# Optimization experiments

Hardware: AMD Instinct MI355X
Metric: run time of the kernel (lower is better)

Reference implementation:

```python
import jax, jax.numpy as jnp
import numpy as np

N_NODES = 100_000
N_EDGES = 1_600_000
F_IN = 64
HID = 128
HEAD_H = 256
OUT = 32
N_GRAPHS = 512
NEG_SLOPE = 0.01  # torch.nn.LeakyReLU default


def _leaky(v):
    return jnp.where(v >= 0, v, NEG_SLOPE * v)


def _gine_layer(x, src, dst, edge_attr, We, be, Wn, bn, n_nodes):
    # GINEConv (eps=0): nn( x_i + sum_j relu(x_j + lin(edge_attr_ji)) )
    msg = jax.nn.relu(x[src] + edge_attr @ We + be)          # [E, in]
    agg = jax.ops.segment_sum(msg, dst, num_segments=n_nodes)  # [N, in]
    return (agg + x) @ Wn + bn                                # [N, hid]


def setup_inputs() -> dict:
    key = jax.random.key(0)
    ks = jax.random.split(key, 24)
    inp = {}
    inp["x"] = jax.random.normal(ks[0], (N_NODES, F_IN), dtype=jnp.float32)
    inp["edge_index"] = jax.random.randint(ks[1], (2, N_EDGES), 0, N_NODES, dtype=jnp.int32)
    inp["edge_attr"] = jax.random.normal(ks[2], (N_EDGES, 2), dtype=jnp.float32)
    inp["batch"] = jnp.sort(jax.random.randint(ks[3], (N_NODES,), 0, N_GRAPHS, dtype=jnp.int32))
    # GINE layers: edge lin (2 -> in) and nn Linear (in -> hid)
    dims = [F_IN, HID, HID]
    ki = 4
    for l, d_in in enumerate(dims):
        inp[f"We{l}"] = jax.random.normal(ks[ki], (2, d_in), dtype=jnp.float32) / np.sqrt(2.0); ki += 1
        inp[f"be{l}"] = jnp.zeros((d_in,), dtype=jnp.float32)
        inp[f"Wn{l}"] = jax.random.normal(ks[ki], (d_in, HID), dtype=jnp.float32) / np.sqrt(d_in); ki += 1
        inp[f"bn{l}"] = jnp.zeros((HID,), dtype=jnp.float32)
    # head MLP
    inp["Wh0"] = jax.random.normal(ks[ki], (HID, HEAD_H), dtype=jnp.float32) / np.sqrt(HID); ki += 1
    inp["bh0"] = jnp.zeros((HEAD_H,), dtype=jnp.float32)
    inp["Wh1"] = jax.random.normal(ks[ki], (HEAD_H, OUT), dtype=jnp.float32) / np.sqrt(HEAD_H); ki += 1
    inp["bh1"] = jnp.zeros((OUT,), dtype=jnp.float32)
    return inp


def reference(x, edge_index, edge_attr, batch,
              We0, be0, Wn0, bn0,
              We1, be1, Wn1, bn1,
              We2, be2, Wn2, bn2,
              Wh0, bh0, Wh1, bh1):
    src, dst = edge_index[0], edge_index[1]
    h = _leaky(_gine_layer(x, src, dst, edge_attr, We0, be0, Wn0, bn0, N_NODES))
    h = _leaky(_gine_layer(h, src, dst, edge_attr, We1, be1, Wn1, bn1, N_NODES))
    h = _leaky(_gine_layer(h, src, dst, edge_attr, We2, be2, Wn2, bn2, N_NODES))
    pooled = jax.ops.segment_sum(h, batch, num_segments=N_GRAPHS)  # [G, HID]
    h = _leaky(pooled @ Wh0 + bh0)
    return h @ Wh1 + bh1  # [G, OUT]
```

## Files before the change

kernel.cpp:

```cpp
#include <hip/hip_runtime.h>
#include <hip/hip_bf16.h>

#define N_NODES 100000
#define N_EDGES 1600000
#define F_IN 64
#define HID 128
#define HEAD_H 256
#define OUT_F 32
#define N_GRAPHS 512
#define NBK 98
#define SLOT 20480
#define BCHUNK 2048
#define NCHUNKS ((N_EDGES + BCHUNK - 1) / BCHUNK)

typedef float f2v __attribute__((ext_vector_type(2)));
typedef short bf16x8 __attribute__((ext_vector_type(8)));
typedef float f32x4 __attribute__((ext_vector_type(4)));

__device__ __forceinline__ float leaky(float v) {
    return v >= 0.f ? v : 0.01f * v;
}

__device__ __forceinline__ float bf2f(ushort u) {
    union { uint i; float f; } c; c.i = ((uint)u) << 16; return c.f;
}

__device__ __forceinline__ ushort f2bf(float f) {
    union { float f; uint i; } c; c.f = f;
    uint r = c.i + 0x7FFF + ((c.i >> 16) & 1);
    return (ushort)(r >> 16);
}

__global__ __launch_bounds__(256) void cast_kernel(const float* __restrict__ x,
                                                   ushort* __restrict__ xb, int n2) {
    int i = blockIdx.x * 256 + threadIdx.x;
    if (i < n2) {
        float2 v = ((const float2*)x)[i];
        uint u = (uint)f2bf(v.x) | ((uint)f2bf(v.y) << 16);
        ((uint*)xb)[i] = u;
    }
}

__global__ __launch_bounds__(256) void prep_wnT(const float* __restrict__ Wn0,
                                                const float* __restrict__ Wn1,
                                                const float* __restrict__ Wn2,
                                                ushort* __restrict__ w0T,
                                                ushort* __restrict__ w1T,
                                                ushort* __restrict__ w2T) {
    int id = blockIdx.x * 256 + threadIdx.x;
    if (id < 128 * 64) {
        int j = id / 64, k = id % 64;
        w0T[id] = f2bf(Wn0[k * 128 + j]);
    } else if (id < 128 * 64 + 128 * 128) {
        int t = id - 128 * 64; int j = t / 128, k = t % 128;
        w1T[t] = f2bf(Wn1[k * 128 + j]);
    } else if (id < 128 * 64 + 2 * 128 * 128) {
        int t = id - 128 * 64 - 128 * 128; int j = t / 128, k = t % 128;
        w2T[t] = f2bf(Wn2[k * 128 + j]);
    }
}


__global__ __launch_bounds__(128) void init_bcur(int* __restrict__ bcur) {
    int t = threadIdx.x;
    if (t < NBK) bcur[t] = t * SLOT;
}

__global__ __launch_bounds__(256) void bin_kernel(const int* __restrict__ src,
                                                  const int* __restrict__ dst,
                                                  const float2* __restrict__ ea,
                                                  int* __restrict__ bcur,
                                                  uint2* __restrict__ recs1) {
    __shared__ int hist[NBK], tmp[NBK], offs[NBK], cur[NBK], gbase[NBK];
    __shared__ uint2 stage[BCHUNK];
    __shared__ unsigned char sbid[BCHUNK];

    int tid = threadIdx.x;
    int e0 = blockIdx.x * BCHUNK;
    int nn = N_EDGES - e0; if (nn > BCHUNK) nn = BCHUNK;

    if (tid < NBK) hist[tid] = 0;
    __syncthreads();

    for (int i = tid; i < nn; i += 256) {
        atomicAdd(&hist[dst[e0 + i] >> 10], 1);
    }
    __syncthreads();

    if (tid < NBK) tmp[tid] = hist[tid];
    __syncthreads();
    for (int off = 1; off < NBK; off <<= 1) {
        int u = (tid < NBK && tid >= off) ? tmp[tid - off] : 0;
        __syncthreads();
        if (tid < NBK) tmp[tid] += u;
        __syncthreads();
    }
    if (tid < NBK) {
        int ex = tmp[tid] - hist[tid];
        offs[tid] = ex;
        cur[tid] = ex;
        gbase[tid] = (hist[tid] > 0) ? atomicAdd(&bcur[tid], hist[tid]) : 0;
    }
    __syncthreads();

    for (int i = tid; i < nn; i += 256) {
        int e = e0 + i;
        int d = dst[e];
        int b = d >> 10;
        int dloc = d & 1023;
        float2 a = ea[e];
        uint2 r;
        r.x = (uint)src[e] | ((uint)dloc << 22);
        r.y = (uint)f2bf(a.x) | ((uint)f2bf(a.y) << 16);
        int pos = atomicAdd(&cur[b], 1);
        stage[pos] = r;
        sbid[pos] = (unsigned char)b;
    }
    __syncthreads();

    for (int i = tid; i < nn; i += 256) {
        int b = sbid[i];
        recs1[gbase[b] + (i - offs[b])] = stage[i];
    }
}

__global__ __launch_bounds__(256) void order_kernel(const uint2* __restrict__ recs1,
                                                    const int* __restrict__ bcur,
                                                    int* __restrict__ rbeg,
                                                    int* __restrict__ rend,
                                                    uint2* __restrict__ recs2) {
    __shared__ int h[1024];
    __shared__ int ssum[256];
    int b = blockIdx.x;
    int tid = threadIdx.x;
    int base = b * SLOT;
    int end = bcur[b];

    for (int i = tid; i < 1024; i += 256) h[i] = 0;
    __syncthreads();

    for (int t = base + tid; t < end; t += 256) {
        atomicAdd(&h[recs1[t].x >> 22], 1);
    }
    __syncthreads();

    int i4 = tid * 4;
    int a0 = h[i4], a1 = h[i4 + 1], a2 = h[i4 + 2], a3 = h[i4 + 3];
    int s = a0 + a1 + a2 + a3;
    ssum[tid] = s;
    __syncthreads();
    for (int off = 1; off < 256; off <<= 1) {
        int u = (tid >= off) ? ssum[tid - off] : 0;
        __syncthreads();
        ssum[tid] += u;
        __syncthreads();
    }
    int pre = base + ssum[tid] - s;
    int c0 = pre, c1 = pre + a0, c2 = c1 + a1, c3 = c2 + a2;
    h[i4] = c0; h[i4 + 1] = c1; h[i4 + 2] = c2; h[i4 + 3] = c3;

    int n = (b << 10) + i4;
    if (n + 4 <= N_NODES) {
        *(int4*)(rbeg + n) = make_int4(c0, c1, c2, c3);
        *(int4*)(rend + n) = make_int4(c0 + a0, c1 + a1, c2 + a2, c3 + a3);
    } else {
        if (n + 0 < N_NODES) { rbeg[n + 0] = c0; rend[n + 0] = c0 + a0; }
        if (n + 1 < N_NODES) { rbeg[n + 1] = c1; rend[n + 1] = c1 + a1; }
        if (n + 2 < N_NODES) { rbeg[n + 2] = c2; rend[n + 2] = c2 + a2; }
        if (n + 3 < N_NODES) { rbeg[n + 3] = c3; rend[n + 3] = c3 + a3; }
    }
    __syncthreads();

    for (int t = base + tid; t < end; t += 256) {
        uint2 r = recs1[t];
        int pos = atomicAdd(&h[r.x >> 22], 1);
        recs2[pos] = make_uint2(r.x & 0x3FFFFFu, r.y);
    }
}


template <int K>
__global__ __launch_bounds__(256) void gine_fused(const ushort* __restrict__ xb,
                                                  const uint2* __restrict__ recs,
                                                  const int* __restrict__ rbeg,
                                                  const int* __restrict__ rend,
                                                  const float* __restrict__ We,
                                                  const float* __restrict__ be,
                                                  const ushort* __restrict__ wnT,
                                                  const float* __restrict__ bn,
                                                  ushort* __restrict__ hb) {
    __shared__ float tile[16 * K];
    __shared__ int node_ctr;
    int tid = threadIdx.x;
    int wave = tid >> 6;
    int lane = tid & 63;
    int n0 = blockIdx.x * 16;

    if (tid == 0) node_ctr = 0;
    __syncthreads();

    if constexpr (K == 128) {
        int j = lane * 2;
        f2v w0v = {We[j], We[j + 1]};
        f2v w1v = {We[128 + j], We[128 + j + 1]};
        f2v bbv = {be[j], be[j + 1]};
        const f2v zero = {0.f, 0.f};

        for (;;) {
            int q = 0;
            if (lane == 0) q = atomicAdd(&node_ctr, 1);
            q = __builtin_amdgcn_readfirstlane(q);
            if (q >= 16) break;
            int node = n0 + q;
            int rs = __builtin_amdgcn_readfirstlane(rbeg[node]);
            int re = __builtin_amdgcn_readfirstlane(rend[node]);
            f2v accv = {0.f, 0.f};

            auto proc = [&](uint2 r, uint u) {
                float ax = bf2f((ushort)(r.y & 0xFFFF));
                float ay = bf2f((ushort)(r.y >> 16));
                union { uint i; float f; } lo, hi;
                lo.i = u << 16;
                hi.i = u & 0xFFFF0000u;
                f2v xv = {lo.f, hi.f};
                f2v m = xv + bbv;
                m = ay * w1v + m;
                m = ax * w0v + m;
                m = __builtin_elementwise_max(m, zero);
                accv += m;
            };

            int t = rs;
            for (; t + 7 < re; t += 8) {
                uint2 r0 = recs[t];
                uint2 r1 = recs[t + 1];
                uint2 r2 = recs[t + 2];
                uint2 r3 = recs[t + 3];
                uint2 r4 = recs[t + 4];
                uint2 r5 = recs[t + 5];
                uint2 r6 = recs[t + 6];
                uint2 r7 = recs[t + 7];
                uint u0 = *(const uint*)(xb + (size_t)r0.x * 128 + j);
                uint u1 = *(const uint*)(xb + (size_t)r1.x * 128 + j);
                uint u2 = *(const uint*)(xb + (size_t)r2.x * 128 + j);
                uint u3 = *(const uint*)(xb + (size_t)r3.x * 128 + j);
                uint u4 = *(const uint*)(xb + (size_t)r4.x * 128 + j);
                uint u5 = *(const uint*)(xb + (size_t)r5.x * 128 + j);
                uint u6 = *(const uint*)(xb + (size_t)r6.x * 128 + j);
                uint u7 = *(const uint*)(xb + (size_t)r7.x * 128 + j);
                proc(r0, u0); proc(r1, u1); proc(r2, u2); proc(r3, u3);
                proc(r4, u4); proc(r5, u5); proc(r6, u6); proc(r7, u7);
            }
            for (; t + 3 < re; t += 4) {
                uint2 r0 = recs[t];
                uint2 r1 = recs[t + 1];
                uint2 r2 = recs[t + 2];
                uint2 r3 = recs[t + 3];
                uint u0 = *(const uint*)(xb + (size_t)r0.x * 128 + j);
                uint u1 = *(const uint*)(xb + (size_t)r1.x * 128 + j);
                uint u2 = *(const uint*)(xb + (size_t)r2.x * 128 + j);
                uint u3 = *(const uint*)(xb + (size_t)r3.x * 128 + j);
                proc(r0, u0); proc(r1, u1); proc(r2, u2); proc(r3, u3);
            }
            for (; t < re; t++) {
                uint2 r0 = recs[t];
                uint u0 = *(const uint*)(xb + (size_t)r0.x * 128 + j);
                proc(r0, u0);
            }

            int idx = (q * 128 + j) ^ ((q & 7) << 2);
            *(f2v*)&tile[idx] = accv;
        }
    } else {
        float w0 = We[lane], w1 = We[64 + lane], bb = be[lane];

        for (;;) {
            int q = 0;
            if (lane == 0) q = atomicAdd(&node_ctr, 1);
            q = __builtin_amdgcn_readfirstlane(q);
            if (q >= 16) break;
            int node = n0 + q;
            int rs = __builtin_amdgcn_readfirstlane(rbeg[node]);
            int re = __builtin_amdgcn_readfirstlane(rend[node]);
            float acc = 0.f;

            auto proc = [&](uint2 r, ushort u) {
                float ax = bf2f((ushort)(r.y & 0xFFFF));
                float ay = bf2f((ushort)(r.y >> 16));
                float m = bf2f(u) + bb;
                m = ay * w1 + m;
                m = ax * w0 + m;
                acc += fmaxf(m, 0.f);
            };

            int t = rs;
            for (; t + 7 < re; t += 8) {
                uint2 r0 = recs[t];
                uint2 r1 = recs[t + 1];
                uint2 r2 = recs[t + 2];
                uint2 r3 = recs[t + 3];
                uint2 r4 = recs[t + 4];
                uint2 r5 = recs[t + 5];
                uint2 r6 = recs[t + 6];
                uint2 r7 = recs[t + 7];
                ushort u0 = xb[(size_t)r0.x * 64 + lane];
                ushort u1 = xb[(size_t)r1.x * 64 + lane];
                ushort u2 = xb[(size_t)r2.x * 64 + lane];
                ushort u3 = xb[(size_t)r3.x * 64 + lane];
                ushort u4 = xb[(size_t)r4.x * 64 + lane];
                ushort u5 = xb[(size_t)r5.x * 64 + lane];
                ushort u6 = xb[(size_t)r6.x * 64 + lane];
                ushort u7 = xb[(size_t)r7.x * 64 + lane];
                proc(r0, u0); proc(r1, u1); proc(r2, u2); proc(r3, u3);
                proc(r4, u4); proc(r5, u5); proc(r6, u6); proc(r7, u7);
            }
            for (; t + 3 < re; t += 4) {
                uint2 r0 = recs[t];
                uint2 r1 = recs[t + 1];
                uint2 r2 = recs[t + 2];
                uint2 r3 = recs[t + 3];
                ushort u0 = xb[(size_t)r0.x * 64 + lane];
                ushort u1 = xb[(size_t)r1.x * 64 + lane];
                ushort u2 = xb[(size_t)r2.x * 64 + lane];
                ushort u3 = xb[(size_t)r3.x * 64 + lane];
                proc(r0, u0); proc(r1, u1); proc(r2, u2); proc(r3, u3);
            }
            for (; t < re; t++) {
                uint2 r0 = recs[t];
                ushort u0 = xb[(size_t)r0.x * 64 + lane];
                proc(r0, u0);
            }

            int idx = (q * 64 + lane) ^ ((q & 7) << 2);
            tile[idx] = acc;
        }
    }
    __syncthreads();

    {
        int l15 = lane & 15;
        int kgrp = (lane >> 4) * 8;
        int row = l15;
        int sw = (row & 7) << 2;
        int nt0 = wave * 2;
        int nt1 = nt0 + 1;
        float b0 = bn[nt0 * 16 + l15];
        float b1 = bn[nt1 * 16 + l15];
        f32x4 acc0 = {b0, b0, b0, b0};
        f32x4 acc1 = {b1, b1, b1, b1};

#pragma unroll
        for (int kk = 0; kk < K / 32; kk++) {
            int k0 = kk * 32 + kgrp;
            f32x4 p0 = *(const f32x4*)&tile[(row * K + k0) ^ sw];
            f32x4 p1 = *(const f32x4*)&tile[(row * K + k0 + 4) ^ sw];
            bf16x8 xr = *(const bf16x8*)(xb + (size_t)(n0 + row) * K + k0);
            bf16x8 a;
#pragma unroll
            for (int e = 0; e < 4; e++) {
                a[e]     = (short)f2bf(p0[e] + bf2f((ushort)xr[e]));
                a[e + 4] = (short)f2bf(p1[e] + bf2f((ushort)xr[e + 4]));
            }
            bf16x8 bf0 = *(const bf16x8*)(wnT + (size_t)(nt0 * 16 + l15) * K + k0);
            bf16x8 bf1 = *(const bf16x8*)(wnT + (size_t)(nt1 * 16 + l15) * K + k0);
            acc0 = __builtin_amdgcn_mfma_f32_16x16x32_bf16(a, bf0, acc0, 0, 0, 0);
            acc1 = __builtin_amdgcn_mfma_f32_16x16x32_bf16(a, bf1, acc1, 0, 0, 0);
        }

        int rbase = n0 + (lane >> 4) * 4;
#pragma unroll
        for (int r = 0; r < 4; r++) {
            hb[(size_t)(rbase + r) * HID + nt0 * 16 + l15] = f2bf(leaky(acc0[r]));
            hb[(size_t)(rbase + r) * HID + nt1 * 16 + l15] = f2bf(leaky(acc1[r]));
        }
    }
}

#define POOL_NPW 64
__global__ __launch_bounds__(256) void pool_kernel(const ushort* __restrict__ h,
                                                   const int* __restrict__ batch,
                                                   float* __restrict__ pooled) {
    int wid = (blockIdx.x * 256 + (int)threadIdx.x) >> 6;
    int lane = threadIdx.x & 63;
    int n0 = wid * POOL_NPW;
    if (n0 >= N_NODES) return;
    int n1 = n0 + POOL_NPW; if (n1 > N_NODES) n1 = N_NODES;

    int j = lane * 2;
    f2v acc = {0.f, 0.f};
    int g = __builtin_amdgcn_readfirstlane(batch[n0]);
    for (int i = n0; i < n1; i++) {
        int bg = __builtin_amdgcn_readfirstlane(batch[i]);
        if (bg != g) {
            atomicAdd(&pooled[g * HID + j], acc.x);
            atomicAdd(&pooled[g * HID + j + 1], acc.y);
            acc.x = 0.f; acc.y = 0.f;
            g = bg;
        }
        uint u = *(const uint*)(h + (size_t)i * HID + j);
        union { uint i; float f; } lo, hi;
        lo.i = u << 16;
        hi.i = u & 0xFFFF0000u;
        acc.x += lo.f;
        acc.y += hi.f;
    }
    atomicAdd(&pooled[g * HID + j], acc.x);
    atomicAdd(&pooled[g * HID + j + 1], acc.y);
}


__global__ __launch_bounds__(256) void head_kernel(const float* __restrict__ pooled,
                                                   const float* __restrict__ Wh0,
                                                   const float* __restrict__ bh0,
                                                   const float* __restrict__ Wh1,
                                                   const float* __restrict__ bh1,
                                                   float* __restrict__ out) {
    __shared__ float p[HID];
    __shared__ float hid[HEAD_H];
    int g = blockIdx.x;
    int t = threadIdx.x;
    if (t < HID) p[t] = pooled[g * HID + t];
    __syncthreads();
    float acc = bh0[t];
    for (int k = 0; k < HID; k++) acc += p[k] * Wh0[k * HEAD_H + t];
    hid[t] = leaky(acc);
    __syncthreads();
    if (t < OUT_F) {
        float o = bh1[t];
        for (int k = 0; k < HEAD_H; k++) o += hid[k] * Wh1[k * OUT_F + t];
        out[g * OUT_F + t] = o;
    }
}

extern "C" void kernel_launch(void* const* d_in, const int* in_sizes, int n_in,
                              void* d_out, int out_size, void* d_ws, size_t ws_size,
                              hipStream_t stream) {
    const float* x     = (const float*)d_in[0];
    const int*   ei    = (const int*)d_in[1];
    const float* ea    = (const float*)d_in[2];
    const int*   batch = (const int*)d_in[3];
    const float* We0 = (const float*)d_in[4];
    const float* be0 = (const float*)d_in[5];
    const float* Wn0 = (const float*)d_in[6];
    const float* bn0 = (const float*)d_in[7];
    const float* We1 = (const float*)d_in[8];
    const float* be1 = (const float*)d_in[9];
    const float* Wn1 = (const float*)d_in[10];
    const float* bn1 = (const float*)d_in[11];
    const float* We2 = (const float*)d_in[12];
    const float* be2 = (const float*)d_in[13];
    const float* Wn2 = (const float*)d_in[14];
    const float* bn2 = (const float*)d_in[15];
    const float* Wh0 = (const float*)d_in[16];
    const float* bh0 = (const float*)d_in[17];
    const float* Wh1 = (const float*)d_in[18];
    const float* bh1 = (const float*)d_in[19];

    const int* src = ei;
    const int* dst = ei + N_EDGES;

    char* ws = (char*)d_ws;
    size_t o = 0;
    uint2*  recs1 = (uint2*)(ws + o); o += (size_t)NBK * SLOT * 8;
    uint2*  recs2 = (uint2*)(ws + o); o += (size_t)NBK * SLOT * 8;
    ushort* xb0  = (ushort*)(ws + o); o += (size_t)N_NODES * 64 * 2;
    ushort* hbufA = (ushort*)(ws + o); o += (size_t)N_NODES * 128 * 2;
    ushort* hbufB = (ushort*)(ws + o); o += (size_t)N_NODES * 128 * 2;
    int*    rbeg = (int*)(ws + o);    o += 400384;
    int*    rend = (int*)(ws + o);    o += 400384;
    int*    bcur = (int*)(ws + o);    o += 4096;
    ushort* wnT0 = (ushort*)(ws + o); o += 128 * 64 * 2;
    ushort* wnT1 = (ushort*)(ws + o); o += 128 * 128 * 2;
    ushort* wnT2 = (ushort*)(ws + o); o += 128 * 128 * 2;
    float*  pooled = (float*)(ws + o); o += (size_t)N_GRAPHS * HID * 4;

    cast_kernel<<<(N_NODES * F_IN / 2 + 255) / 256, 256, 0, stream>>>(x, xb0, N_NODES * F_IN / 2);
    prep_wnT<<<160, 256, 0, stream>>>(Wn0, Wn1, Wn2, wnT0, wnT1, wnT2);

    init_bcur<<<1, 128, 0, stream>>>(bcur);
    bin_kernel<<<NCHUNKS, 256, 0, stream>>>(src, dst, (const float2*)ea, bcur, recs1);
    order_kernel<<<NBK, 256, 0, stream>>>(recs1, bcur, rbeg, rend, recs2);

    const int FUSED_BLOCKS = N_NODES / 16;

    gine_fused<64><<<FUSED_BLOCKS, 256, 0, stream>>>(xb0, recs2, rbeg, rend, We0, be0, wnT0, bn0, hbufA);
    gine_fused<128><<<FUSED_BLOCKS, 256, 0, stream>>>(hbufA, recs2, rbeg, rend, We1, be1, wnT1, bn1, hbufB);
    gine_fused<128><<<FUSED_BLOCKS, 256, 0, stream>>>(hbufB, recs2, rbeg, rend, We2, be2, wnT2, bn2, hbufA);

    hipMemsetAsync(pooled, 0, (size_t)N_GRAPHS * HID * sizeof(float), stream);
    pool_kernel<<<(N_NODES / POOL_NPW + 3) / 4, 256, 0, stream>>>(hbufA, batch, pooled);
    head_kernel<<<N_GRAPHS, 256, 0, stream>>>(pooled, Wh0, bh0, Wh1, bh1, (float*)d_out);
}
```

Baseline: 340.0 us.

## Merge setup kernels, vectorize binning loads, interleave row ranges, prefetch next node

Merges the cast and weight-transpose kernels into one launch and replaces the init_bcur kernel with a memset, storing bucket cursors as relative offsets. The binning kernel now loads dst, src and edge_attr as 4-wide vectors. Row begin and end are interleaved into one array, and the fused GINE kernels fetch the next work-stolen node's range before processing the current one. The aim is fewer launches and less memory latency, at the cost of more complex indexing and alignment assumptions on vector loads.

```diff
diff --git a/kernel.cpp b/kernel.cpp
--- a/kernel.cpp
+++ b/kernel.cpp
@@ -12,6 +12,7 @@
 #define SLOT 20480
 #define BCHUNK 2048
 #define NCHUNKS ((N_EDGES + BCHUNK - 1) / BCHUNK)
+#define CAST_BLOCKS (N_NODES * F_IN / 2 / 256)
 
 typedef float f2v __attribute__((ext_vector_type(2)));
 typedef short bf16x8 __attribute__((ext_vector_type(8)));
@@ -31,40 +32,35 @@
     return (ushort)(r >> 16);
 }
 
-__global__ __launch_bounds__(256) void cast_kernel(const float* __restrict__ x,
-                                                   ushort* __restrict__ xb, int n2) {
-    int i = blockIdx.x * 256 + threadIdx.x;
-    if (i < n2) {
+__global__ __launch_bounds__(256) void setup_kernel(const float* __restrict__ x,
+                                                    ushort* __restrict__ xb,
+                                                    const float* __restrict__ Wn0,
+                                                    const float* __restrict__ Wn1,
+                                                    const float* __restrict__ Wn2,
+                                                    ushort* __restrict__ w0T,
+                                                    ushort* __restrict__ w1T,
+                                                    ushort* __restrict__ w2T) {
+    int b = blockIdx.x;
+    if (b < CAST_BLOCKS) {
+        int i = b * 256 + threadIdx.x;
         float2 v = ((const float2*)x)[i];
         uint u = (uint)f2bf(v.x) | ((uint)f2bf(v.y) << 16);
         ((uint*)xb)[i] = u;
-    }
-}
-
-__global__ __launch_bounds__(256) void prep_wnT(const float* __restrict__ Wn0,
-                                                const float* __restrict__ Wn1,
-                                                const float* __restrict__ Wn2,
-                                                ushort* __restrict__ w0T,
-                                                ushort* __restrict__ w1T,
-                                                ushort* __restrict__ w2T) {
-    int id = blockIdx.x * 256 + threadIdx.x;
-    if (id < 128 * 64) {
-        int j = id / 64, k = id % 64;
-        w0T[id] = f2bf(Wn0[k * 128 + j]);
-    } else if (id < 128 * 64 + 128 * 128) {
-        int t = id - 128 * 64; int j = t / 128, k = t % 128;
-        w1T[t] = f2bf(Wn1[k * 128 + j]);
-    } else if (id < 128 * 64 + 2 * 128 * 128) {
-        int t = id - 128 * 64 - 128 * 128; int j = t / 128, k = t % 128;
-        w2T[t] = f2bf(Wn2[k * 128 + j]);
-    }
-}
-
-
-__global__ __launch_bounds__(128) void init_bcur(int* __restrict__ bcur) {
-    int t = threadIdx.x;
-    if (t < NBK) bcur[t] = t * SLOT;
-}
+    } else {
+        int id = (b - CAST_BLOCKS) * 256 + threadIdx.x;
+        if (id < 128 * 64) {
+            int j = id / 64, k = id % 64;
+            w0T[id] = f2bf(Wn0[k * 128 + j]);
+        } else if (id < 128 * 64 + 128 * 128) {
+            int t = id - 128 * 64; int j = t / 128, k = t % 128;
+            w1T[t] = f2bf(Wn1[k * 128 + j]);
+        } else if (id < 128 * 64 + 2 * 128 * 128) {
+            int t = id - 128 * 64 - 128 * 128; int j = t / 128, k = t % 128;
+            w2T[t] = f2bf(Wn2[k * 128 + j]);
+        }
+    }
+}
+
 
 __global__ __launch_bounds__(256) void bin_kernel(const int* __restrict__ src,
                                                   const int* __restrict__ dst,
@@ -82,8 +78,12 @@
     if (tid < NBK) hist[tid] = 0;
     __syncthreads();
 
-    for (int i = tid; i < nn; i += 256) {
-        atomicAdd(&hist[dst[e0 + i] >> 10], 1);
+    for (int i0 = tid * 4; i0 < nn; i0 += 1024) {
+        int4 d4 = *(const int4*)(dst + e0 + i0);
+        atomicAdd(&hist[d4.x >> 10], 1);
+        atomicAdd(&hist[d4.y >> 10], 1);
+        atomicAdd(&hist[d4.z >> 10], 1);
+        atomicAdd(&hist[d4.w >> 10], 1);
     }
     __syncthreads();
 
@@ -99,22 +99,30 @@
         int ex = tmp[tid] - hist[tid];
         offs[tid] = ex;
         cur[tid] = ex;
-        gbase[tid] = (hist[tid] > 0) ? atomicAdd(&bcur[tid], hist[tid]) : 0;
-    }
-    __syncthreads();
-
-    for (int i = tid; i < nn; i += 256) {
-        int e = e0 + i;
-        int d = dst[e];
-        int b = d >> 10;
-        int dloc = d & 1023;
-        float2 a = ea[e];
-        uint2 r;
-        r.x = (uint)src[e] | ((uint)dloc << 22);
-        r.y = (uint)f2bf(a.x) | ((uint)f2bf(a.y) << 16);
-        int pos = atomicAdd(&cur[b], 1);
-        stage[pos] = r;
-        sbid[pos] = (unsigned char)b;
+        gbase[tid] = (hist[tid] > 0) ? (tid * SLOT + atomicAdd(&bcur[tid], hist[tid])) : 0;
+    }
+    __syncthreads();
+
+    for (int i0 = tid * 4; i0 < nn; i0 += 1024) {
+        int e = e0 + i0;
+        int4 d4 = *(const int4*)(dst + e);
+        int4 s4 = *(const int4*)(src + e);
+        float4 ea01 = *(const float4*)(ea + e);
+        float4 ea23 = *(const float4*)(ea + e + 2);
+#pragma unroll
+        for (int k = 0; k < 4; k++) {
+            int d = (k == 0) ? d4.x : (k == 1) ? d4.y : (k == 2) ? d4.z : d4.w;
+            int s = (k == 0) ? s4.x : (k == 1) ? s4.y : (k == 2) ? s4.z : s4.w;
+            float aex = (k == 0) ? ea01.x : (k == 1) ? ea01.z : (k == 2) ? ea23.x : ea23.z;
+            float aey = (k == 0) ? ea01.y : (k == 1) ? ea01.w : (k == 2) ? ea23.y : ea23.w;
+            int b = d >> 10;
+            uint2 r;
+            r.x = (uint)s | ((uint)(d & 1023) << 22);
+            r.y = (uint)f2bf(aex) | ((uint)f2bf(aey) << 16);
+            int pos = atomicAdd(&cur[b], 1);
+            stage[pos] = r;
+            sbid[pos] = (unsigned char)b;
+        }
     }
     __syncthreads();
 
@@ -126,15 +134,14 @@
 
 __global__ __launch_bounds__(256) void order_kernel(const uint2* __restrict__ recs1,
                                                     const int* __restrict__ bcur,
-                                                    int* __restrict__ rbeg,
-                                                    int* __restrict__ rend,
+                                                    int* __restrict__ rr,
                                                     uint2* __restrict__ recs2) {
     __shared__ int h[1024];
     __shared__ int ssum[256];
     int b = blockIdx.x;
     int tid = threadIdx.x;
     int base = b * SLOT;
-    int end = bcur[b];
+    int end = base + bcur[b];
 
     for (int i = tid; i < 1024; i += 256) h[i] = 0;
     __syncthreads();
@@ -161,13 +168,13 @@
 
     int n = (b << 10) + i4;
     if (n + 4 <= N_NODES) {
-        *(int4*)(rbeg + n) = make_int4(c0, c1, c2, c3);
-        *(int4*)(rend + n) = make_int4(c0 + a0, c1 + a1, c2 + a2, c3 + a3);
+        *(int4*)(rr + 2 * n)     = make_int4(c0, c0 + a0, c1, c1 + a1);
+        *(int4*)(rr + 2 * n + 4) = make_int4(c2, c2 + a2, c3, c3 + a3);
     } else {
-        if (n + 0 < N_NODES) { rbeg[n + 0] = c0; rend[n + 0] = c0 + a0; }
-        if (n + 1 < N_NODES) { rbeg[n + 1] = c1; rend[n + 1] = c1 + a1; }
-        if (n + 2 < N_NODES) { rbeg[n + 2] = c2; rend[n + 2] = c2 + a2; }
-        if (n + 3 < N_NODES) { rbeg[n + 3] = c3; rend[n + 3] = c3 + a3; }
+        if (n + 0 < N_NODES) { rr[2 * n + 0] = c0; rr[2 * n + 1] = c0 + a0; }
+        if (n + 1 < N_NODES) { rr[2 * n + 2] = c1; rr[2 * n + 3] = c1 + a1; }
+        if (n + 2 < N_NODES) { rr[2 * n + 4] = c2; rr[2 * n + 5] = c2 + a2; }
+        if (n + 3 < N_NODES) { rr[2 * n + 6] = c3; rr[2 * n + 7] = c3 + a3; }
     }
     __syncthreads();
 
@@ -182,8 +189,7 @@
 template <int K>
 __global__ __launch_bounds__(256) void gine_fused(const ushort* __restrict__ xb,
                                                   const uint2* __restrict__ recs,
-                                                  const int* __restrict__ rbeg,
-                                                  const int* __restrict__ rend,
+                                                  const int* __restrict__ rr,
                                                   const float* __restrict__ We,
                                                   const float* __restrict__ be,
                                                   const ushort* __restrict__ wnT,
@@ -199,6 +205,12 @@
     if (tid == 0) node_ctr = 0;
     __syncthreads();
 
+    auto steal = [&]() -> int {
+        int q = 0;
+        if (lane == 0) q = atomicAdd(&node_ctr, 1);
+        return __builtin_amdgcn_readfirstlane(q);
+    };
+
     if constexpr (K == 128) {
         int j = lane * 2;
         f2v w0v = {We[j], We[j + 1]};
@@ -206,14 +218,19 @@
         f2v bbv = {be[j], be[j + 1]};
         const f2v zero = {0.f, 0.f};
 
-        for (;;) {
-            int q = 0;
-            if (lane == 0) q = atomicAdd(&node_ctr, 1);
-            q = __builtin_amdgcn_readfirstlane(q);
-            if (q >= 16) break;
-            int node = n0 + q;
-            int rs = __builtin_amdgcn_readfirstlane(rbeg[node]);
-            int re = __builtin_amdgcn_readfirstlane(rend[node]);
+        int q = steal();
+        int rs = 0, re = 0;
+        if (q < 16) {
+            rs = __builtin_amdgcn_readfirstlane(rr[2 * (n0 + q)]);
+            re = __builtin_amdgcn_readfirstlane(rr[2 * (n0 + q) + 1]);
+        }
+        while (q < 16) {
+            int q2 = steal();
+            int rs2 = 0, re2 = 0;
+            if (q2 < 16) {
+                rs2 = __builtin_amdgcn_readfirstlane(rr[2 * (n0 + q2)]);
+                re2 = __builtin_amdgcn_readfirstlane(rr[2 * (n0 + q2) + 1]);
+            }
             f2v accv = {0.f, 0.f};
 
             auto proc = [&](uint2 r, uint u) {
@@ -270,18 +287,24 @@
 
             int idx = (q * 128 + j) ^ ((q & 7) << 2);
             *(f2v*)&tile[idx] = accv;
+            q = q2; rs = rs2; re = re2;
         }
     } else {
         float w0 = We[lane], w1 = We[64 + lane], bb = be[lane];
 
-        for (;;) {
-            int q = 0;
-            if (lane == 0) q = atomicAdd(&node_ctr, 1);
-            q = __builtin_amdgcn_readfirstlane(q);
-            if (q >= 16) break;
-            int node = n0 + q;
-            int rs = __builtin_amdgcn_readfirstlane(rbeg[node]);
-            int re = __builtin_amdgcn_readfirstlane(rend[node]);
+        int q = steal();
+        int rs = 0, re = 0;
+        if (q < 16) {
+            rs = __builtin_amdgcn_readfirstlane(rr[2 * (n0 + q)]);
+            re = __builtin_amdgcn_readfirstlane(rr[2 * (n0 + q) + 1]);
+        }
+        while (q < 16) {
+            int q2 = steal();
+            int rs2 = 0, re2 = 0;
+            if (q2 < 16) {
+                rs2 = __builtin_amdgcn_readfirstlane(rr[2 * (n0 + q2)]);
+                re2 = __builtin_amdgcn_readfirstlane(rr[2 * (n0 + q2) + 1]);
+            }
             float acc = 0.f;
 
             auto proc = [&](uint2 r, ushort u) {
@@ -333,6 +356,7 @@
 
             int idx = (q * 64 + lane) ^ ((q & 7) << 2);
             tile[idx] = acc;
+            q = q2; rs = rs2; re = re2;
         }
     }
     __syncthreads();
@@ -466,26 +490,24 @@
     ushort* xb0  = (ushort*)(ws + o); o += (size_t)N_NODES * 64 * 2;
     ushort* hbufA = (ushort*)(ws + o); o += (size_t)N_NODES * 128 * 2;
     ushort* hbufB = (ushort*)(ws + o); o += (size_t)N_NODES * 128 * 2;
-    int*    rbeg = (int*)(ws + o);    o += 400384;
-    int*    rend = (int*)(ws + o);    o += 400384;
+    int*    rr   = (int*)(ws + o);    o += (size_t)N_NODES * 8 + 768;
     int*    bcur = (int*)(ws + o);    o += 4096;
     ushort* wnT0 = (ushort*)(ws + o); o += 128 * 64 * 2;
     ushort* wnT1 = (ushort*)(ws + o); o += 128 * 128 * 2;
     ushort* wnT2 = (ushort*)(ws + o); o += 128 * 128 * 2;
     float*  pooled = (float*)(ws + o); o += (size_t)N_GRAPHS * HID * 4;
 
-    cast_kernel<<<(N_NODES * F_IN / 2 + 255) / 256, 256, 0, stream>>>(x, xb0, N_NODES * F_IN / 2);
-    prep_wnT<<<160, 256, 0, stream>>>(Wn0, Wn1, Wn2, wnT0, wnT1, wnT2);
-
-    init_bcur<<<1, 128, 0, stream>>>(bcur);
+    setup_kernel<<<CAST_BLOCKS + 160, 256, 0, stream>>>(x, xb0, Wn0, Wn1, Wn2, wnT0, wnT1, wnT2);
+
+    hipMemsetAsync(bcur, 0, NBK * sizeof(int), stream);
     bin_kernel<<<NCHUNKS, 256, 0, stream>>>(src, dst, (const float2*)ea, bcur, recs1);
-    order_kernel<<<NBK, 256, 0, stream>>>(recs1, bcur, rbeg, rend, recs2);
+    order_kernel<<<NBK, 256, 0, stream>>>(recs1, bcur, rr, recs2);
 
     const int FUSED_BLOCKS = N_NODES / 16;
 
-    gine_fused<64><<<FUSED_BLOCKS, 256, 0, stream>>>(xb0, recs2, rbeg, rend, We0, be0, wnT0, bn0, hbufA);
-    gine_fused<128><<<FUSED_BLOCKS, 256, 0, stream>>>(hbufA, recs2, rbeg, rend, We1, be1, wnT1, bn1, hbufB);
-    gine_fused<128><<<FUSED_BLOCKS, 256, 0, stream>>>(hbufB, recs2, rbeg, rend, We2, be2, wnT2, bn2, hbufA);
+    gine_fused<64><<<FUSED_BLOCKS, 256, 0, stream>>>(xb0, recs2, rr, We0, be0, wnT0, bn0, hbufA);
+    gine_fused<128><<<FUSED_BLOCKS, 256, 0, stream>>>(hbufA, recs2, rr, We1, be1, wnT1, bn1, hbufB);
+    gine_fused<128><<<FUSED_BLOCKS, 256, 0, stream>>>(hbufB, recs2, rr, We2, be2, wnT2, bn2, hbufA);
 
     hipMemsetAsync(pooled, 0, (size_t)N_GRAPHS * HID * sizeof(float), stream);
     pool_kernel<<<(N_NODES / POOL_NPW + 3) / 4, 256, 0, stream>>>(hbufA, batch, pooled);
```

Measured after the change: 343.0 us. About the same (+0.9%).
